# Kernel tuning notes

Measured on AMD Instinct MI355X. Metric: run time of the kernel, lower is better.

The kernel has to match this reference:

```python
import jax, jax.numpy as jnp
import numpy as np


def _lstm_step(x, h, c, wx, wh, b):
    # Keras LSTMCell gate order: i, f, g(candidate), o
    z = x @ wx + h @ wh + b
    i, f, g, o = jnp.split(z, 4, axis=-1)
    c2 = jax.nn.sigmoid(f) * c + jax.nn.sigmoid(i) * jnp.tanh(g)
    h2 = jax.nn.sigmoid(o) * jnp.tanh(c2)
    return h2, c2


def setup_inputs() -> dict:
    key = jax.random.key(0)
    ks = jax.random.split(key, 16)
    B, S, T = 64, 256, 500
    n_mel, E, P, A, D, AD, F, K = 80, 512, 256, 1024, 1024, 128, 32, 31
    g = lambda i, shape, s=0.02: jax.random.normal(ks[i], shape, jnp.float32) * s
    return {
        'memory': g(0, (B, S, E), 1.0),
        'mel_inputs': g(1, (B, T, n_mel), 1.0),
        'prenet_w1': g(2, (n_mel, P)),
        'prenet_w2': g(3, (P, P)),
        'att_lstm_wx': g(4, (P + E, 4 * A)),
        'att_lstm_wh': g(5, (A, 4 * A)),
        'att_lstm_b': jnp.zeros((4 * A,), jnp.float32),
        'w_query': g(6, (A, AD)),
        'w_memory': g(7, (E, AD)),
        'loc_conv': g(8, (K, 2, F)),
        'w_loc': g(9, (F, AD)),
        'v_att': g(10, (AD,)),
        'dec_lstm_wx': g(11, (A + E, 4 * D)),
        'dec_lstm_wh': g(12, (D, 4 * D)),
        'dec_lstm_b': jnp.zeros((4 * D,), jnp.float32),
        'proj_w': g(13, (D + E, n_mel)),
        'proj_b': jnp.zeros((n_mel,), jnp.float32),
        'gate_w': g(14, (D + E, 1)),
        'gate_b': jnp.zeros((1,), jnp.float32),
    }


def reference(memory, mel_inputs, prenet_w1, prenet_w2,
              att_lstm_wx, att_lstm_wh, att_lstm_b,
              w_query, w_memory, loc_conv, w_loc, v_att,
              dec_lstm_wx, dec_lstm_wh, dec_lstm_b,
              proj_w, proj_b, gate_w, gate_b):
    B, S, E = memory.shape
    A = att_lstm_wh.shape[0]
    D = dec_lstm_wh.shape[0]
    # keys computed once (memory layer of LSA)
    keys = memory @ w_memory  # [B, S, AD]

    def step(carry, mel_in):
        h_a, c_a, h_d, c_d, ctx, w, w_cum = carry
        # Prenet (deterministic: dropout disabled, no bias, relu)
        p = jax.nn.relu(jax.nn.relu(mel_in @ prenet_w1) @ prenet_w2)
        # Attention RNN
        x = jnp.concatenate([p, ctx], axis=-1)
        h_a, c_a = _lstm_step(x, h_a, c_a, att_lstm_wx, att_lstm_wh, att_lstm_b)
        # Location-sensitive attention
        loc = jnp.stack([w, w_cum], axis=-1)  # [B, S, 2]
        f = jax.lax.conv_general_dilated(
            loc, loc_conv, window_strides=(1,), padding='SAME',
            dimension_numbers=('NWC', 'WIO', 'NWC'))  # [B, S, F]
        e = jnp.tanh((h_a @ w_query)[:, None, :] + keys + f @ w_loc) @ v_att  # [B, S]
        w_new = jax.nn.softmax(e, axis=-1)
        ctx_new = jnp.einsum('bs,bse->be', w_new, memory)
        w_cum_new = w_cum + w_new
        # Decoder RNN (stacked, n=1)
        y = jnp.concatenate([h_a, ctx_new], axis=-1)
        h_d, c_d = _lstm_step(y, h_d, c_d, dec_lstm_wx, dec_lstm_wh, dec_lstm_b)
        cat = jnp.concatenate([h_d, ctx_new], axis=-1)
        mel = cat @ proj_w + proj_b
        stop = jax.nn.sigmoid(cat @ gate_w + gate_b)
        new_carry = (h_a, c_a, h_d, c_d, ctx_new, w_new, w_cum_new)
        return new_carry, (mel, stop, w_new)

    z = jnp.zeros
    carry0 = (z((B, A)), z((B, A)), z((B, D)), z((B, D)),
              z((B, E)), z((B, S)), z((B, S)))
    _, (mels, stops, aligns) = jax.lax.scan(step, carry0,
                                            jnp.swapaxes(mel_inputs, 0, 1))
    # [T,B,*] -> [B,T,*]
    return (jnp.swapaxes(mels, 0, 1), jnp.swapaxes(stops, 0, 1),
            jnp.swapaxes(aligns, 0, 1))
```

## Files before the change

kernel.cpp:

```cpp
#include <hip/hip_runtime.h>
#include <hip/hip_cooperative_groups.h>

namespace cg = cooperative_groups;

constexpr int NB   = 64;
constexpr int NS   = 256;
constexpr int NT   = 500;
constexpr int NMEL = 80;
constexpr int NE   = 512;
constexpr int NP   = 256;
constexpr int NA   = 1024;
constexpr int ND   = 1024;
constexpr int NAD  = 128;
constexpr int ZC   = 4096;
constexpr int KA   = 1792;
constexpr int KD   = 2560;
constexpr int NKA  = 11;
constexpr int NKD  = 16;
constexpr int G    = 512;

constexpr int SMN  = 5280;

constexpr int OFF_KEYST = 0;
constexpr int OFF_FL    = OFF_KEYST + NB * NAD * NS;
// ... 21 lines not shown
constexpr long M2_HA   = M2_ZDP + 2 * NB * ZC;
constexpr long M2_CA   = M2_HA + NB * NA;
constexpr long M2_HD   = M2_CA + NB * NA;
constexpr long M2_CD   = M2_HD + NB * ND;
constexpr long M2_CTX  = M2_CD + NB * ND;
constexpr long M2_WGL  = M2_CTX + 2 * NB * NE;
constexpr long M2_WCU  = M2_WGL + NB * NS;
constexpr long M2_PM1  = M2_WCU + NB * NS;
constexpr long M2_ZCNT = M2_PM1 - M2_HA;
constexpr long M2_BAR  = M2_PM1 + NB * NP;
constexpr long M2_FEND = M2_BAR + 1024;
constexpr long M2_WAT   = 0;
constexpr long M2_WDT   = M2_WAT + (long)ZC * KA;
constexpr long M2_X16A  = M2_WDT + (long)ZC * KD;
constexpr long M2_X16D  = M2_X16A + (long)NB * KA;
constexpr long M2_K16   = M2_X16D + (long)NB * KD;
constexpr long M2_FL16  = M2_K16 + (long)NB * NAD * NS;
constexpr long M2_MEM16 = M2_FL16 + (long)NB * NAD * NS;
constexpr long M2_UEND_NM = M2_MEM16;
constexpr long M2_UEND    = M2_MEM16 + (long)NB * NS * NE;
constexpr long M2_BYTES_NM = M2_FEND * 4 + M2_UEND_NM * 2;
constexpr long M2_BYTES    = M2_FEND * 4 + M2_UEND * 2;

constexpr int G3 = 256, T3 = 512;
constexpr long M3_W2   = 0;
constexpr long M3_ZA   = M3_W2 + 62 * NAD;
constexpr long M3_ZD   = M3_ZA + NB * ZC;
constexpr long M3_CTX  = M3_ZD + NB * ZC;
constexpr long M3_WGL  = M3_CTX + 2 * NB * NE;
constexpr long M3_WCU  = M3_WGL + NB * NS;
constexpr long M3_PM1  = M3_WCU + NB * NS;
constexpr long M3_BAR  = M3_PM1 + NB * NP;
constexpr long M3_FEND = M3_BAR + 1024;
constexpr long M3_WAT  = 0;
constexpr long M3_WDT  = M3_WAT + (long)ZC * KA;
constexpr long M3_X16A = M3_WDT + (long)ZC * KD;
constexpr long M3_X16D = M3_X16A + (long)NB * KA;
constexpr long M3_K16  = M3_X16D + (long)NB * KD;
constexpr long M3_FL16 = M3_K16 + (long)NB * NAD * NS;
constexpr long M3_WQ16 = M3_FL16 + (long)NB * NAD * NS;
constexpr long M3_MEMT = M3_WQ16 + (long)NA * NAD;
constexpr long M3_UEND = M3_MEMT + (long)NB * NE * NS;
constexpr long M3_BYTES = M3_FEND * 4 + M3_UEND * 2;
constexpr int  DYN_LDS  = 159744;

constexpr long MEL_BASE   = 0;
constexpr long STOP_BASE  = (long)NB * NT * NMEL;
constexpr long ALIGN_BASE = STOP_BASE + (long)NB * NT;

typedef __attribute__((ext_vector_type(8))) short bf16x8;
typedef __attribute__((ext_vector_type(4))) float f32x4;

struct Params {
  const float *memory, *mel, *pw1, *pw2, *awx, *awh, *ab, *wq, *wm,
              *lconv, *wloc, *vatt, *dwx, *dwh, *db, *projw, *projb, *gatew, *gateb;
  float *out, *ws;
};

__device__ __forceinline__ float sigm(float x) { return 1.f / (1.f + __expf(-x)); }
__device__ __forceinline__ float tanh_t(float x) {
  x = fminf(fmaxf(x, -15.f), 15.f);
  const float a = __expf(2.f * x);
  return (a - 1.f) / (a + 1.f);
}
__device__ __forceinline__ unsigned short f2bf(float x) {
  union { float f; unsigned u; } c; c.f = x;
  const unsigned r = c.u + 0x7FFFu + ((c.u >> 16) & 1u);
  return (unsigned short)(r >> 16);
}
__device__ __forceinline__ float bf2f(unsigned short v) {
  union { unsigned u; float f; } c; c.u = (unsigned)v << 16;
  return c.f;
}

__device__ __forceinline__ void gbar(unsigned* bar, int wg, int tid) {
  __syncthreads();
  if (tid == 0) {
    unsigned* gen  = bar;
    unsigned* root = bar + 32;
    unsigned* leaf = bar + 64 + (wg >> 5) * 32;
    const unsigned g = __hip_atomic_load(gen, __ATOMIC_RELAXED, __HIP_MEMORY_SCOPE_AGENT);
    __threadfence();
    const unsigned lo = __hip_atomic_fetch_add(leaf, 1u, __ATOMIC_ACQ_REL,
                                               __HIP_MEMORY_SCOPE_AGENT);
    if (lo == 31) {
      __hip_atomic_store(leaf, 0u, __ATOMIC_RELAXED, __HIP_MEMORY_SCOPE_AGENT);
      const unsigned ro = __hip_atomic_fetch_add(root, 1u, __ATOMIC_ACQ_REL,
                                                 __HIP_MEMORY_SCOPE_AGENT);
      if (ro == 15) {
        __hip_atomic_store(root, 0u, __ATOMIC_RELAXED, __HIP_MEMORY_SCOPE_AGENT);
        __hip_atomic_fetch_add(gen, 1u, __ATOMIC_ACQ_REL, __HIP_MEMORY_SCOPE_AGENT);
      }
    }
    while (__hip_atomic_load(gen, __ATOMIC_RELAXED, __HIP_MEMORY_SCOPE_AGENT) == g)
      __builtin_amdgcn_s_sleep(16);
// ... 8 lines not shown
    unsigned* gen  = bar;
    unsigned* root = bar + 32;
    unsigned* leaf = bar + 64 + (wg >> 4) * 32;
    const unsigned g = __hip_atomic_load(gen, __ATOMIC_RELAXED, __HIP_MEMORY_SCOPE_AGENT);
    __threadfence();
    const unsigned lo = __hip_atomic_fetch_add(leaf, 1u, __ATOMIC_ACQ_REL,
                                               __HIP_MEMORY_SCOPE_AGENT);
    if (lo == 15) {
      __hip_atomic_store(leaf, 0u, __ATOMIC_RELAXED, __HIP_MEMORY_SCOPE_AGENT);
      const unsigned ro = __hip_atomic_fetch_add(root, 1u, __ATOMIC_ACQ_REL,
                                                 __HIP_MEMORY_SCOPE_AGENT);
      if (ro == 15) {
        __hip_atomic_store(root, 0u, __ATOMIC_RELAXED, __HIP_MEMORY_SCOPE_AGENT);
        __hip_atomic_fetch_add(gen, 1u, __ATOMIC_ACQ_REL, __HIP_MEMORY_SCOPE_AGENT);
      }
    }
    while (__hip_atomic_load(gen, __ATOMIC_RELAXED, __HIP_MEMORY_SCOPE_AGENT) == g)
      __builtin_amdgcn_s_sleep(8);
    __threadfence();
  }
  __syncthreads();
}

__device__ void do_s1(const Params& p, float* pm1, int tnext, int wl, int tid) {
  const int col = tid;
  for (int i = 0; i < 8; ++i) {
    const int b = wl * 8 + i;
    const float* mrow = p.mel + ((size_t)b * NT + tnext) * NMEL;
    float acc = 0.f;
    for (int k = 0; k < NMEL; ++k) acc += mrow[k] * p.pw1[k * NP + col];
    pm1[b * NP + col] = fmaxf(acc, 0.f);
  }
}

template<int MODE>
__device__ void do_s2(const Params& p, const float* pm1, float* pdst,
                      unsigned short* xA, int wl, int tid) {
  const int col = tid;
  for (int i = 0; i < 4; ++i) {
    const int b = wl * 4 + i;
    const float* pr = pm1 + b * NP;
    float acc = 0.f;
    for (int k = 0; k < NP; ++k) acc += pr[k] * p.pw2[k * NP + col];
    const float v = fmaxf(acc, 0.f);
    if constexpr (MODE >= 2) xA[(size_t)b * KA + col] = f2bf(v);
    else                     pdst[b * NP + col] = v;
  }
}

__device__ void do_fl3(const Params& p, float* scr, unsigned short* u16, int wg, int tid) {
  float* ws = p.ws;
  float* chunk = scr;
  float* wp = scr + 3968;
  const int hf = tid >> 8, ts = tid & 255;
  const int b = (wg - 144) * 2 + hf;
  float* wp0 = wp + hf * 576;
  float* wp1 = wp0 + 288;
  for (int i = ts; i < 288; i += 256) { wp0[i] = 0.f; wp1[i] = 0.f; }
  __syncthreads();
  wp0[15 + ts] = ws[M3_WGL + b * NS + ts];
  wp1[15 + ts] = ws[M3_WCU + b * NS + ts];
  __syncthreads();
  float x0[31], x1[31];
#pragma unroll
  for (int k = 0; k < 31; ++k) { x0[k] = wp0[ts + k]; x1[k] = wp1[ts + k]; }
  const unsigned short* kb16 = u16 + M3_K16 + (size_t)(b * NAD) * NS + ts;
  unsigned short* fb16 = u16 + M3_FL16 + (size_t)(b * NAD) * NS + ts;
  const float* W2g = ws + M3_W2;
  for (int ch = 0; ch < 2; ++ch) {
    for (int i = tid; i < 62 * 64; i += T3) {
      const int k2 = i >> 6, adl = i & 63;
      chunk[i] = W2g[k2 * NAD + ch * 64 + adl];
    }
    __syncthreads();
    for (int adl = 0; adl < 64; ++adl) {
      const int ad = ch * 64 + adl;
      float acc = bf2f(kb16[(size_t)ad * NS]);
#pragma unroll
      for (int k = 0; k < 31; ++k)
        acc = fmaf(x0[k], chunk[(2 * k) * 64 + adl],
              fmaf(x1[k], chunk[(2 * k + 1) * 64 + adl], acc));
      fb16[(size_t)ad * NS] = f2bf(acc);
    }
    __syncthreads();
  }
}

__device__ void attn3(const Params& p, float* scr, unsigned short* u16,
                      int b, int tid, int t, float& c0, float& c1) {
  if (t >= NT) return;
  float* ws = p.ws;
  float* h_sh = scr;
  float* red  = scr + 1024;
  float* q_sh = scr + 1536;
  float* w_sh = scr + 1664;
  unsigned short* xA = u16 + M3_X16A + (size_t)b * KA;
  unsigned short* xD = u16 + M3_X16D + (size_t)b * KD;
  const float* za = ws + M3_ZA + (size_t)b * ZC;
#pragma unroll
  for (int j = 0; j < 2; ++j) {
    const int g = tid + j * 512;
    const float zi = p.ab[g] + za[g];
    const float zf = p.ab[1024 + g] + za[1024 + g];
    const float zg = p.ab[2048 + g] + za[2048 + g];
    const float zo = p.ab[3072 + g] + za[3072 + g];
    float& cc = j ? c1 : c0;
    const float iv = sigm(zi), fv = sigm(zf), gv = tanh_t(zg), ov = sigm(zo);
    const float cn = fv * cc + iv * gv;
    const float h2 = ov * tanh_t(cn);
    cc = cn;
    h_sh[g] = h2;
    xA[768 + g] = f2bf(h2);
    xD[g]       = f2bf(h2);
  }
  __syncthreads();
  {
    const int ad = tid & 127, kh = tid >> 7;
    const unsigned short* wqp = u16 + M3_WQ16 + ad;
    float acc = 0.f;
#pragma unroll 16
    for (int k = kh * 256; k < kh * 256 + 256; ++k) acc += h_sh[k] * bf2f(wqp[(size_t)k * NAD]);
    red[tid] = acc;
  }
  __syncthreads();
  if (tid < 128) q_sh[tid] = red[tid] + red[tid + 128] + red[tid + 256] + red[tid + 384];
  __syncthreads();
  float evp = 0.f;
  {
    const int s = tid & 255, hf = tid >> 8;
    const unsigned short* flp = u16 + M3_FL16 + (size_t)(b * NAD + hf * 64) * NS + s;
    const float* qs = q_sh + hf * 64;
    const float* va = p.vatt + hf * 64;
#pragma unroll 8
    for (int ad = 0; ad < 64; ++ad)
      evp += tanh_t(qs[ad] + bf2f(flp[(size_t)ad * NS])) * va[ad];
  }
  red[tid] = evp;
  __syncthreads();
  float evs = 0.f;
  if (tid < 256) evs = red[tid] + red[tid + 256];
  __syncthreads();
  if (tid < 256) red[tid] = evs;
  __syncthreads();
  for (int off = 128; off > 0; off >>= 1) {
    if (tid < off) red[tid] = fmaxf(red[tid], red[tid + off]);
    __syncthreads();
  }
  const float mx = red[0];
  __syncthreads();
  const float ex = (tid < 256) ? __expf(evs - mx) : 0.f;
  red[tid] = ex;
  __syncthreads();
  for (int off = 128; off > 0; off >>= 1) {
    if (tid < off) red[tid] += red[tid + off];
    __syncthreads();
  }
  const float sden = red[0];
  if (tid < 256) {
    const float wv = ex / sden;
    w_sh[tid] = wv;
    ws[M3_WGL + b * NS + tid] = wv;
    ws[M3_WCU + b * NS + tid] += wv;
    p.out[ALIGN_BASE + (size_t)b * NT * NS + (size_t)t * NS + tid] = wv;
  }
  __syncthreads();
  {
    const int e = tid;
    const unsigned short* mrow = u16 + M3_MEMT + ((size_t)b * NE + e) * NS;
    float a0 = 0.f;
#pragma unroll 4
    for (int sc = 0; sc < 32; ++sc) {
      const bf16x8 v = *(const bf16x8*)(mrow + sc * 8);
#pragma unroll
      for (int j = 0; j < 8; ++j) a0 += w_sh[sc * 8 + j] * bf2f((unsigned short)v[j]);
    }
    float* cdst = ws + M3_CTX + (t & 1) * (NB * NE) + b * NE;
    cdst[e] = a0;
    xA[256 + e]  = f2bf(a0);
    xD[1024 + e] = f2bf(a0);
  }
}

__device__ void dec3(const Params& p, float* scr, unsigned short* u16,
                     int b, int tid, int t, float& c0, float& c1) {
  if (t < 1) return;
  const int tm1 = t - 1;
  float* ws = p.ws;
  float* h_sh = scr;
  float* red  = scr + 1024;
  unsigned short* xD = u16 + M3_X16D + (size_t)b * KD;
  const float* zd = ws + M3_ZD + (size_t)b * ZC;
#pragma unroll
  for (int j = 0; j < 2; ++j) {
    const int g = tid + j * 512;
    const float zi = p.db[g] + zd[g];
    const float zf = p.db[1024 + g] + zd[1024 + g];
    const float zg = p.db[2048 + g] + zd[2048 + g];
    const float zo = p.db[3072 + g] + zd[3072 + g];
    float& cc = j ? c1 : c0;
    const float iv = sigm(zi), fv = sigm(zf), gv = tanh_t(zg), ov = sigm(zo);
    const float cn = fv * cc + iv * gv;
    const float h2 = ov * tanh_t(cn);
    cc = cn;
    h_sh[g] = h2;
    xD[1536 + g] = f2bf(h2);
  }
  __syncthreads();
  const float* ctxf = ws + M3_CTX + (tm1 & 1) * (NB * NE) + b * NE;
  red[tid] = h_sh[tid] * p.gatew[tid] + h_sh[tid + 512] * p.gatew[tid + 512]
           + ctxf[tid] * p.gatew[tid + 1024];
  __syncthreads();
  for (int off = 256; off > 0; off >>= 1) {
    if (tid < off) red[tid] += red[tid + off];
    __syncthreads();
  }
  if (tid == 0) p.out[STOP_BASE + (size_t)b * NT + tm1] = sigm(red[0] + p.gateb[0]);
  __syncthreads();
  if (tid < 480) {
    const int m = tid % 80, kh = tid / 80;
    float acc = 0.f;
#pragma unroll 8
    for (int k = kh * 256; k < kh * 256 + 256; ++k) {
      const float v = (k < 1024) ? h_sh[k] : ctxf[k - 1024];
      acc += v * p.projw[(size_t)k * 80 + m];
    }
    red[kh * 80 + m] = acc;
  }
  __syncthreads();
  if (tid < 80) {
    float mval = p.projb[tid];
#pragma unroll
    for (int kh = 0; kh < 6; ++kh) mval += red[kh * 80 + tid];
    p.out[MEL_BASE + (size_t)b * NT * NMEL + (size_t)tm1 * NMEL + tid] = mval;
  }
}

__global__ __launch_bounds__(512, 1) void taco3(Params p) {
  cg::grid_group grid = cg::this_grid();
  const int wg = blockIdx.x, tid = threadIdx.x;
  extern __shared__ char dynsm[];
  unsigned short* wA_l = (unsigned short*)dynsm;
  unsigned short* wD_l = (unsigned short*)(dynsm + 57344);
  float* scr = (float*)(dynsm + 139264);
  float* ws = p.ws;
  unsigned short* u16 = (unsigned short*)(ws + M3_FEND);

  {
    const long gid = (long)wg * T3 + tid, gstr = (long)G3 * T3;
    for (long i = gid; i < 98304; i += gstr) ws[M3_CTX + i] = 0.f;
    if (wg == 0) for (int i = tid; i < 1024; i += T3) ((unsigned*)(ws + M3_BAR))[i] = 0;
    for (long i = gid; i < 62 * NAD; i += gstr) {
      const int k2 = (int)(i >> 7), ad = (int)(i & 127);
      float a = 0.f;
      for (int f = 0; f < 32; ++f) a += p.lconv[k2 * 32 + f] * p.wloc[f * NAD + ad];
      ws[M3_W2 + i] = a;
    }
    for (long i = gid; i < (long)NB * KA + (long)NB * KD; i += gstr) u16[M3_X16A + i] = 0;
    for (long i = gid; i < (long)NA * NAD; i += gstr) u16[M3_WQ16 + i] = f2bf(p.wq[i]);
    for (long i = gid; i < (long)NB * NE * NS; i += gstr) {
      const int s = (int)(i & 255);
      const long be = i >> 8;
      const int e = (int)(be & 511), b = (int)(be >> 9);
      u16[M3_MEMT + i] = f2bf(p.memory[((size_t)b * NS + s) * NE + e]);
    }
    {
      const int b = wg >> 2, s0 = (wg & 3) * 64;
      const int sl = tid & 31, adg = tid >> 5;
      const float* wmb = p.wm + adg * 8;
      for (int so = 0; so < 64; so += 32) {
        const float* mrow = p.memory + (size_t)(b * NS + s0 + so + sl) * NE;
        float acc[8];
#pragma unroll
        for (int j = 0; j < 8; ++j) acc[j] = 0.f;
        for (int k = 0; k < NE; ++k) {
          const float mv = mrow[k];
          const float* wr = wmb + (size_t)k * NAD;
#pragma unroll
          for (int j = 0; j < 8; ++j) acc[j] += mv * wr[j];
        }
#pragma unroll
        for (int j = 0; j < 8; ++j)
          u16[M3_K16 + (size_t)(b * NAD + adg * 8 + j) * NS + s0 + so + sl] = f2bf(acc[j]);
      }
    }
    for (int tile = wg; tile < 3584 + 5120; tile += G3) {
      const bool iA = tile < 3584;
      const int tt = iA ? tile : tile - 3584;
      const int NKB = iA ? 56 : 80;
      const int nt4 = tt / NKB, kb = tt % NKB;
      const int kx = iA ? 768 : 1536;
      float4 v0{}, v1{};
      if (tid < 256) {
        const int r = tid >> 3, cgp = (tid & 7) * 8;
        const int k = kb * 32 + r;
        const float* src = iA
            ? (k < kx ? p.awx + (size_t)k * ZC : p.awh + (size_t)(k - kx) * ZC)
            : (k < kx ? p.dwx + (size_t)k * ZC : p.dwh + (size_t)(k - kx) * ZC);
        const float* sp = src + nt4 * 64 + cgp;
        v0 = *(const float4*)sp;
        v1 = *(const float4*)(sp + 4);
      }
      __syncthreads();
      if (tid < 256) {
        const int r = tid >> 3, cgp = (tid & 7) * 8;
        *(float4*)(scr + r * 64 + cgp)     = v0;
        *(float4*)(scr + r * 64 + cgp + 4) = v1;
      }
      __syncthreads();
      if (tid < 256) {
        const int blk = tid >> 6, l = tid & 63;
        const int n16 = nt4 * 4 + blk;
        bf16x8 pk;
#pragma unroll
        for (int j = 0; j < 8; ++j)
          pk[j] = (short)f2bf(scr[((l >> 4) * 8 + j) * 64 + blk * 16 + (l & 15)]);
        unsigned short* dst = u16 + (iA ? M3_WAT : M3_WDT)
                            + ((size_t)(n16 * NKB + kb)) * 512 + l * 8;
        *(bf16x8*)dst = pk;
      }
      __syncthreads();
    }
    if (wg >= 176 && wg < 184 && tid < 256) do_s1(p, ws + M3_PM1, 0, wg - 176, tid);
  }
  grid.sync();
  {
    const float4* srcA = (const float4*)(u16 + M3_WAT + (size_t)wg * 56 * 512);
    float4* dA = (float4*)wA_l;
    for (int i = tid; i < 3584; i += T3) dA[i] = srcA[i];
    const float4* srcD = (const float4*)(u16 + M3_WDT + (size_t)wg * 80 * 512);
    float4* dD = (float4*)wD_l;
    for (int i = tid; i < 5120; i += T3) dD[i] = srcD[i];
    if (wg >= 128 && wg < 144 && tid < 256)
      do_s2<3>(p, ws + M3_PM1, nullptr, u16 + M3_X16A, wg - 128, tid);
  }
  grid.sync();

  float c0 = 0.f, c1 = 0.f;
  unsigned* bar = (unsigned*)(ws + M3_BAR);
  for (int t = 0; t <= NT; ++t) {
    {
      const int wid = tid >> 6, l = tid & 63;
      if (wid < 4) {
        if (t < NT) {
          const unsigned short* xb = u16 + M3_X16A
              + (size_t)(wid * 16 + (l & 15)) * KA + (l >> 4) * 8;
          f32x4 acc{0.f, 0.f, 0.f, 0.f};
#pragma unroll 8
          for (int ks = 0; ks < 56; ++ks) {
            const bf16x8 bfr = *(const bf16x8*)(wA_l + ks * 512 + l * 8);
            const bf16x8 a   = *(const bf16x8*)(xb + ks * 32);
            acc = __builtin_amdgcn_mfma_f32_16x16x32_bf16(a, bfr, acc, 0, 0, 0);
          }
          const int ncol = wg * 16 + (l & 15), rb = (l >> 4) * 4;
          float* z = ws + M3_ZA;
#pragma unroll
          for (int r = 0; r < 4; ++r) z[(size_t)(wid * 16 + rb + r) * ZC + ncol] = acc[r];
        }
      } else {
        if (t >= 1) {
          const int mb = wid - 4;
          const unsigned short* xb = u16 + M3_X16D
              + (size_t)(mb * 16 + (l & 15)) * KD + (l >> 4) * 8;
          f32x4 acc{0.f, 0.f, 0.f, 0.f};
#pragma unroll 8
          for (int ks = 0; ks < 80; ++ks) {
            const bf16x8 bfr = *(const bf16x8*)(wD_l + ks * 512 + l * 8);
            const bf16x8 a   = *(const bf16x8*)(xb + ks * 32);
            acc = __builtin_amdgcn_mfma_f32_16x16x32_bf16(a, bfr, acc, 0, 0, 0);
          }
          const int ncol = wg * 16 + (l & 15), rb = (l >> 4) * 4;
          float* z = ws + M3_ZD;
#pragma unroll
          for (int r = 0; r < 4; ++r) z[(size_t)(mb * 16 + rb + r) * ZC + ncol] = acc[r];
        }
      }
      if (wg >= 144 && wg < 176) {
        if (t < NT) do_fl3(p, scr, u16, wg, tid);
      } else if (wg >= 176 && wg < 184) {
        if (t + 1 < NT && tid < 256) do_s1(p, ws + M3_PM1, t + 1, wg - 176, tid);
      }
    }
    gbar3(bar, wg, tid);
    if (wg < 64)       attn3(p, scr, u16, wg, tid, t, c0, c1);
    else if (wg < 128) dec3(p, scr, u16, wg - 64, tid, t, c0, c1);
    else if (wg < 144) {
      if (t + 1 < NT && tid < 256)
        do_s2<3>(p, ws + M3_PM1, nullptr, u16 + M3_X16A, wg - 128, tid);
    }
    gbar3(bar, wg, tid);
  }
}

template<bool USEMEM>
__device__ void pre_a2(const Params& p, float* sm, int wg, int tid) {
  float* ws = p.ws;
  unsigned short* u16 = (unsigned short*)(ws + M2_FEND);
  const long gid = wg * 256 + tid;
  const long gstr = (long)G * 256;
  for (long i = gid; i < M2_ZCNT; i += gstr) (ws + M2_HA)[i] = 0.f;
  if (wg == 0) for (int i = tid; i < 1024; i += 256) ((unsigned*)(ws + M2_BAR))[i] = 0;
  for (long i = gid; i < 62 * NAD; i += gstr) {
    const int k2 = (int)(i >> 7), ad = (int)(i & 127);
    float acc = 0.f;
    for (int f = 0; f < 32; ++f) acc += p.lconv[k2 * 32 + f] * p.wloc[f * NAD + ad];
    ws[M2_W2 + i] = acc;
  }
  {
    const int b = wg >> 3, s0 = (wg & 7) * 32;
    const int sl = tid & 31, adg = tid >> 5;
    const float* mrow = p.memory + (size_t)(b * NS + s0 + sl) * NE;
// ... 25 lines not shown
    const int kx = iA ? 768 : 1536;
    const int r = tid >> 3, cgp = (tid & 7) * 8;
    const int k = kb * 32 + r;
    const float* src = iA
        ? (k < kx ? p.awx + (size_t)k * ZC : p.awh + (size_t)(k - kx) * ZC)
        : (k < kx ? p.dwx + (size_t)k * ZC : p.dwh + (size_t)(k - kx) * ZC);
    const float* sp = src + nt4 * 64 + cgp;
    const float4 v0 = *(const float4*)sp;
    const float4 v1 = *(const float4*)(sp + 4);
    __syncthreads();
    *(float4*)(sm + r * 64 + cgp)     = v0;
    *(float4*)(sm + r * 64 + cgp + 4) = v1;
    __syncthreads();
    const int blk = tid >> 6, l = tid & 63;
    const int n16 = nt4 * 4 + blk;
    bf16x8 pk;
#pragma unroll
    for (int j = 0; j < 8; ++j)
      pk[j] = (short)f2bf(sm[((l >> 4) * 8 + j) * 64 + blk * 16 + (l & 15)]);
    unsigned short* dst = u16 + (iA ? M2_WAT : M2_WDT)
                        + ((size_t)(n16 * NKB + kb)) * 512 + l * 8;
    *(bf16x8*)dst = pk;
  }
  if (wg >= 320 && wg < 328) do_s1(p, ws + M2_PM1, 0, wg - 320, tid);
}

__device__ void do_fl2(const Params& p, float* sm, int b, int tid) {
  float* ws = p.ws;
  unsigned short* u16 = (unsigned short*)(ws + M2_FEND);
  float* chunk = sm;
  float* wp0 = sm + 4000;
  float* wp1 = sm + 4320;
  for (int i = tid; i < 288; i += 256) { wp0[i] = 0.f; wp1[i] = 0.f; }
  __syncthreads();
  wp0[15 + tid] = ws[M2_WGL + b * NS + tid];
  wp1[15 + tid] = ws[M2_WCU + b * NS + tid];
  __syncthreads();
  float x0[31], x1[31];
#pragma unroll
  for (int k = 0; k < 31; ++k) { x0[k] = wp0[tid + k]; x1[k] = wp1[tid + k]; }
  const unsigned short* kb16 = u16 + M2_K16 + (size_t)(b * NAD) * NS + tid;
  unsigned short* fb16 = u16 + M2_FL16 + (size_t)(b * NAD) * NS + tid;
  const float* W2g = ws + M2_W2;
  for (int ch = 0; ch < 2; ++ch) {
    for (int i = tid; i < 62 * 64; i += 256) {
      const int k2 = i >> 6, adl = i & 63;
      chunk[i] = W2g[k2 * NAD + ch * 64 + adl];
// ... 37 lines not shown
#pragma unroll 4
      for (int ks = 0; ks < nks; ++ks) {
        const bf16x8 bfr = *(const bf16x8*)(wb + (size_t)ks * 512);
        const bf16x8 a0 = *(const bf16x8*)(xb + ks * 32);
        const bf16x8 a1 = *(const bf16x8*)(xb + ks * 32 + (size_t)16 * Kp);
        const bf16x8 a2 = *(const bf16x8*)(xb + ks * 32 + (size_t)32 * Kp);
        const bf16x8 a3 = *(const bf16x8*)(xb + ks * 32 + (size_t)48 * Kp);
        acc[0] = __builtin_amdgcn_mfma_f32_16x16x32_bf16(a0, bfr, acc[0], 0, 0, 0);
        acc[1] = __builtin_amdgcn_mfma_f32_16x16x32_bf16(a1, bfr, acc[1], 0, 0, 0);
        acc[2] = __builtin_amdgcn_mfma_f32_16x16x32_bf16(a2, bfr, acc[2], 0, 0, 0);
        acc[3] = __builtin_amdgcn_mfma_f32_16x16x32_bf16(a3, bfr, acc[3], 0, 0, 0);
      }
      const int ncol = n16 * 16 + (l & 15);
      const int rb = (l >> 4) * 4;
#pragma unroll
      for (int mb = 0; mb < 4; ++mb)
#pragma unroll
        for (int r = 0; r < 4; ++r)
          zout[(size_t)(mb * 16 + rb + r) * ZC + ncol] = acc[mb][r];
    }
  } else if (wg < 320) {
    if (t < NT) do_fl2(p, sm, wg - 256, tid);
  } else if (wg < 328) {
    if (t + 1 < NT) do_s1(p, ws + M2_PM1, t + 1, wg - 320, tid);
  }
}

template<bool USEMEM>
__device__ void phase2_2(const Params& p, float* sm, int wg, int tid, int t) {
  float* ws = p.ws;
  unsigned short* u16 = (unsigned short*)(ws + M2_FEND);
  if (wg < 64) {
    if (t < NT) {
      const int b = wg;
      float* h_sh = sm;
      float* q_sh = sm + 1024;
      float* red  = sm + 1152;
      float* w_sh = sm + 1408;
      float* c_a  = ws + M2_CA;
      float* h_a  = ws + M2_HA;
      unsigned short* xA = u16 + M2_X16A + (size_t)b * KA;
      unsigned short* xD = u16 + M2_X16D + (size_t)b * KD;
      const float* za0 = ws + M2_ZAP + (size_t)b * ZC;
      const float* za1 = za0 + (size_t)NB * ZC;
#pragma unroll
      for (int j = 0; j < 4; ++j) {
        const int g = tid + j * 256;
// ... 180 lines not shown
    const int k2 = i >> 7, ad = i & 127;
    float acc = 0.f;
    for (int f = 0; f < 32; ++f) acc += p.lconv[k2 * 32 + f] * p.wloc[f * NAD + ad];
    ws[OFF_W2 + i] = acc;
  }
  {
    const int b = wg >> 3, s0 = (wg & 7) * 32;
    const int sl = tid & 31, adg = tid >> 5;
    const float* mrow = p.memory + (size_t)(b * NS + s0 + sl) * NE;
    const float* wmb  = p.wm + adg * 16;
    float acc[16];
#pragma unroll
    for (int j = 0; j < 16; ++j) acc[j] = 0.f;
    for (int k = 0; k < NE; ++k) {
      const float mv = mrow[k];
      const float* wr = wmb + (size_t)k * NAD;
#pragma unroll
      for (int j = 0; j < 16; ++j) acc[j] += mv * wr[j];
    }
#pragma unroll
    for (int j = 0; j < 16; ++j)
      ws[OFF_KEYST + (b * NAD + adg * 16 + j) * NS + s0 + sl] = acc[j];
  }
  if (wg >= 496 && wg < 504) do_s1(p, ws + OFF_PM1, 0, wg - 496, tid);
}

__device__ void do_fl(const Params& p, float* sm, int b, int tid) {
  float* ws = p.ws;
  float* chunk = sm;
  float* wp0 = sm + 4000;
  float* wp1 = sm + 4320;
  for (int i = tid; i < 288; i += 256) { wp0[i] = 0.f; wp1[i] = 0.f; }
  __syncthreads();
  wp0[15 + tid] = ws[OFF_WGL + b * NS + tid];
  wp1[15 + tid] = ws[OFF_WCU + b * NS + tid];
  __syncthreads();
  float x0[31], x1[31];
#pragma unroll
  for (int k = 0; k < 31; ++k) { x0[k] = wp0[tid + k]; x1[k] = wp1[tid + k]; }
  const float* kb = ws + OFF_KEYST + (b * NAD) * NS + tid;
  float* fb = ws + OFF_FL + (b * NAD) * NS + tid;
  const float* W2g = ws + OFF_W2;
  for (int ch = 0; ch < 2; ++ch) {
    for (int i = tid; i < 62 * 64; i += 256) {
      const int k2 = i >> 6, adl = i & 63;
      chunk[i] = W2g[k2 * NAD + ch * 64 + adl];
    }
// ... 126 lines not shown
      if constexpr (MODE == 1) {
        float* zdp = ws + OFF_ZDP;
#pragma unroll
        for (int i = 0; i < 8; ++i) {
          const int b = b0 + bgrp * 8 + i;
          float* dst = zdp + (size_t)(kci * NB + b) * ZC + c;
          *(float4*)dst       = make_float4(acc[i][0], acc[i][1], acc[i][2], acc[i][3]);
          *(float4*)(dst + 4) = make_float4(acc[i][4], acc[i][5], acc[i][6], acc[i][7]);
        }
      } else {
        float* z_d = ws + OFF_ZD;
#pragma unroll
        for (int i = 0; i < 8; ++i) {
          const int b = b0 + bgrp * 8 + i;
#pragma unroll
          for (int j = 0; j < 8; ++j) atomicAdd(&z_d[b * ZC + c + j], acc[i][j]);
        }
      }
      __syncthreads();
    }
  } else if (wg < 496) {
    if (t < NT) do_fl(p, sm, wg - 432, tid);
  } else if (wg < 504) {
    if (t + 1 < NT) do_s1(p, ws + OFF_PM1, t + 1, wg - 496, tid);
  }
}

template<int MODE>
__device__ void phase2(const Params& p, float* sm, int wg, int tid, int t) {
  float* ws = p.ws;
  if (wg < 64) {
    if (t < NT) {
      const int b = wg;
      float* h_sh = sm;
      float* q_sh = sm + 1024;
      float* red  = sm + 1152;
      float* w_sh = sm + 1408;
      float* c_a  = ws + OFF_CA;
      float* h_a  = ws + OFF_HA;
#pragma unroll
      for (int j = 0; j < 4; ++j) {
        const int g = tid + j * 256;
        float zi, zf, zg, zo;
        if constexpr (MODE == 1) {
          zi = p.ab[g]; zf = p.ab[1024 + g]; zg = p.ab[2048 + g]; zo = p.ab[3072 + g];
          const float* zap = ws + OFF_ZAP + (size_t)b * ZC;
#pragma unroll 1
// ... 189 lines not shown
  prm.mel    = (const float*)d_in[1];
  prm.pw1    = (const float*)d_in[2];
  prm.pw2    = (const float*)d_in[3];
  prm.awx    = (const float*)d_in[4];
  prm.awh    = (const float*)d_in[5];
  prm.ab     = (const float*)d_in[6];
  prm.wq     = (const float*)d_in[7];
  prm.wm     = (const float*)d_in[8];
  prm.lconv  = (const float*)d_in[9];
  prm.wloc   = (const float*)d_in[10];
  prm.vatt   = (const float*)d_in[11];
  prm.dwx    = (const float*)d_in[12];
  prm.dwh    = (const float*)d_in[13];
  prm.db     = (const float*)d_in[14];
  prm.projw  = (const float*)d_in[15];
  prm.projb  = (const float*)d_in[16];
  prm.gatew  = (const float*)d_in[17];
  prm.gateb  = (const float*)d_in[18];
  prm.out = (float*)d_out;
  prm.ws  = (float*)d_ws;

  void* args[] = { &prm };
  hipError_t err = hipErrorUnknown;
  if (ws_size >= (size_t)M3_BYTES) {
    (void)hipFuncSetAttribute((const void*)taco3,
                              hipFuncAttributeMaxDynamicSharedMemorySize, DYN_LDS);
    err = hipLaunchCooperativeKernel((void*)taco3, dim3(G3), dim3(T3),
                                     args, DYN_LDS, stream);
  }
  if (err != hipSuccess && ws_size >= (size_t)M2_BYTES)
    err = hipLaunchCooperativeKernel((void*)taco2<true>, dim3(G), dim3(256), args, 0, stream);
  if (err != hipSuccess && ws_size >= (size_t)M2_BYTES_NM)
    err = hipLaunchCooperativeKernel((void*)taco2<false>, dim3(G), dim3(256), args, 0, stream);
  if (err != hipSuccess && ws_size >= (size_t)WS_FULL * sizeof(float))
    err = hipLaunchCooperativeKernel((void*)taco_coop<1>, dim3(G), dim3(256), args, 0, stream);
  if (err != hipSuccess)
    err = hipLaunchCooperativeKernel((void*)taco_coop<0>, dim3(G), dim3(256), args, 0, stream);
  if (err != hipSuccess) {
    k_pre_a<<<dim3(G), dim3(256), 0, stream>>>(prm);
    k_pre_b<<<dim3(G), dim3(256), 0, stream>>>(prm);
    for (int t = 0; t <= NT; ++t) {
      k_p1<<<dim3(G), dim3(256), 0, stream>>>(prm, t);
      k_p2<<<dim3(G), dim3(256), 0, stream>>>(prm, t);
    }
  }
}
```

Before: 97.25 ms.

## Transpose keys, location features, query and projection weights for vectorized contiguous access

Stores keys and location features as [B,S,AD] so each thread reads and writes 8 contiguous bf16 values with vector loads, rather than strided scalar accesses. Also pre-transposes w_query and proj_w in setup so the query and mel-projection dot products read contiguous memory, and raises unroll factors on the MFMA and context loops. Adds atomic-load/store helpers for a new MODE 4 that nothing calls yet. The setup phase gains two extra transposition passes and the workspace grows slightly.

```diff
diff --git a/kernel.cpp b/kernel.cpp
--- a/kernel.cpp
+++ b/kernel.cpp
@@ -67,26 +67,27 @@
 constexpr long M2_BYTES_NM = M2_FEND * 4 + M2_UEND_NM * 2;
 constexpr long M2_BYTES    = M2_FEND * 4 + M2_UEND * 2;
 
-constexpr int G3 = 256, T3 = 512;
-constexpr long M3_W2   = 0;
-constexpr long M3_ZA   = M3_W2 + 62 * NAD;
-constexpr long M3_ZD   = M3_ZA + NB * ZC;
-constexpr long M3_CTX  = M3_ZD + NB * ZC;
-constexpr long M3_WGL  = M3_CTX + 2 * NB * NE;
-constexpr long M3_WCU  = M3_WGL + NB * NS;
-constexpr long M3_PM1  = M3_WCU + NB * NS;
-constexpr long M3_BAR  = M3_PM1 + NB * NP;
-constexpr long M3_FEND = M3_BAR + 1024;
-constexpr long M3_WAT  = 0;
-constexpr long M3_WDT  = M3_WAT + (long)ZC * KA;
-constexpr long M3_X16A = M3_WDT + (long)ZC * KD;
-constexpr long M3_X16D = M3_X16A + (long)NB * KA;
-constexpr long M3_K16  = M3_X16D + (long)NB * KD;
-constexpr long M3_FL16 = M3_K16 + (long)NB * NAD * NS;
-constexpr long M3_WQ16 = M3_FL16 + (long)NB * NAD * NS;
-constexpr long M3_MEMT = M3_WQ16 + (long)NA * NAD;
-constexpr long M3_UEND = M3_MEMT + (long)NB * NE * NS;
-constexpr long M3_BYTES = M3_FEND * 4 + M3_UEND * 2;
+constexpr int G5 = 256, T5 = 512;
+constexpr long M5_W2     = 0;
+constexpr long M5_ZA     = M5_W2 + 62 * NAD;
+constexpr long M5_ZD     = M5_ZA + NB * ZC;
+constexpr long M5_CTX    = M5_ZD + NB * ZC;
+constexpr long M5_WGL    = M5_CTX + 2 * NB * NE;
+constexpr long M5_WCU    = M5_WGL + NB * NS;
+constexpr long M5_PM1    = M5_WCU + NB * NS;
+constexpr long M5_PROJWT = M5_PM1 + NB * NP;
+constexpr long M5_BAR    = M5_PROJWT + 80 * 1536;
+constexpr long M5_FEND   = M5_BAR + 1024;
+constexpr long M5_WAT   = 0;
+constexpr long M5_WDT   = M5_WAT + (long)ZC * KA;
+constexpr long M5_X16A  = M5_WDT + (long)ZC * KD;
+constexpr long M5_X16D  = M5_X16A + (long)NB * KA;
+constexpr long M5_K16T  = M5_X16D + (long)NB * KD;
+constexpr long M5_FL16T = M5_K16T + (long)NB * NS * NAD;
+constexpr long M5_WQT   = M5_FL16T + (long)NB * NS * NAD;
+constexpr long M5_MEMT  = M5_WQT + (long)NAD * NA;
+constexpr long M5_UEND  = M5_MEMT + (long)NB * NE * NS;
+constexpr long M5_BYTES = M5_FEND * 4 + M5_UEND * 2;
 constexpr int  DYN_LDS  = 159744;
 
 constexpr long MEL_BASE   = 0;
@@ -116,6 +117,15 @@
 __device__ __forceinline__ float bf2f(unsigned short v) {
   union { unsigned u; float f; } c; c.u = (unsigned)v << 16;
   return c.f;
+}
+__device__ __forceinline__ float ldf(const float* p) {
+  return __hip_atomic_load(p, __ATOMIC_RELAXED, __HIP_MEMORY_SCOPE_AGENT);
+}
+__device__ __forceinline__ void stf(float* p, float v) {
+  __hip_atomic_store(p, v, __ATOMIC_RELAXED, __HIP_MEMORY_SCOPE_AGENT);
+}
+__device__ __forceinline__ void stw(unsigned short* p, unsigned short v) {
+  __hip_atomic_store(p, v, __ATOMIC_RELAXED, __HIP_MEMORY_SCOPE_AGENT);
 }
 
 __device__ __forceinline__ void gbar(unsigned* bar, int wg, int tid) {
@@ -170,6 +180,7 @@
   __syncthreads();
 }
 
+template<int MODE>
 __device__ void do_s1(const Params& p, float* pm1, int tnext, int wl, int tid) {
   const int col = tid;
   for (int i = 0; i < 8; ++i) {
@@ -177,7 +188,8 @@
     const float* mrow = p.mel + ((size_t)b * NT + tnext) * NMEL;
     float acc = 0.f;
     for (int k = 0; k < NMEL; ++k) acc += mrow[k] * p.pw1[k * NP + col];
-    pm1[b * NP + col] = fmaxf(acc, 0.f);
+    if constexpr (MODE == 4) stf(&pm1[b * NP + col], fmaxf(acc, 0.f));
+    else                     pm1[b * NP + col] = fmaxf(acc, 0.f);
   }
 }
 
@@ -189,52 +201,67 @@
     const int b = wl * 4 + i;
     const float* pr = pm1 + b * NP;
     float acc = 0.f;
-    for (int k = 0; k < NP; ++k) acc += pr[k] * p.pw2[k * NP + col];
+    if constexpr (MODE == 4) {
+      for (int k = 0; k < NP; ++k) acc += ldf(&pr[k]) * p.pw2[k * NP + col];
+    } else {
+      for (int k = 0; k < NP; ++k) acc += pr[k] * p.pw2[k * NP + col];
+    }
     const float v = fmaxf(acc, 0.f);
-    if constexpr (MODE >= 2) xA[(size_t)b * KA + col] = f2bf(v);
-    else                     pdst[b * NP + col] = v;
-  }
-}
-
-__device__ void do_fl3(const Params& p, float* scr, unsigned short* u16, int wg, int tid) {
+    if constexpr (MODE == 4)      stw(&xA[(size_t)b * KA + col], f2bf(v));
+    else if constexpr (MODE >= 2) xA[(size_t)b * KA + col] = f2bf(v);
+    else                          pdst[b * NP + col] = v;
+  }
+}
+
+__device__ void do_fl5(const Params& p, float* scr, unsigned short* u16, int wg, int tid) {
   float* ws = p.ws;
   float* chunk = scr;
   float* wp = scr + 3968;
-  const int hf = tid >> 8, ts = tid & 255;
+  const int hf = tid >> 8, s = tid & 255;
   const int b = (wg - 144) * 2 + hf;
   float* wp0 = wp + hf * 576;
   float* wp1 = wp0 + 288;
-  for (int i = ts; i < 288; i += 256) { wp0[i] = 0.f; wp1[i] = 0.f; }
-  __syncthreads();
-  wp0[15 + ts] = ws[M3_WGL + b * NS + ts];
-  wp1[15 + ts] = ws[M3_WCU + b * NS + ts];
+  for (int i = s; i < 288; i += 256) { wp0[i] = 0.f; wp1[i] = 0.f; }
+  __syncthreads();
+  wp0[15 + s] = ws[M5_WGL + b * NS + s];
+  wp1[15 + s] = ws[M5_WCU + b * NS + s];
   __syncthreads();
   float x0[31], x1[31];
 #pragma unroll
-  for (int k = 0; k < 31; ++k) { x0[k] = wp0[ts + k]; x1[k] = wp1[ts + k]; }
-  const unsigned short* kb16 = u16 + M3_K16 + (size_t)(b * NAD) * NS + ts;
-  unsigned short* fb16 = u16 + M3_FL16 + (size_t)(b * NAD) * NS + ts;
-  const float* W2g = ws + M3_W2;
+  for (int k = 0; k < 31; ++k) { x0[k] = wp0[s + k]; x1[k] = wp1[s + k]; }
+  const unsigned short* kb = u16 + M5_K16T + ((size_t)(b * NS + s)) * NAD;
+  unsigned short* fb = u16 + M5_FL16T + ((size_t)(b * NS + s)) * NAD;
+  const float* W2g = ws + M5_W2;
   for (int ch = 0; ch < 2; ++ch) {
-    for (int i = tid; i < 62 * 64; i += T3) {
+    for (int i = tid; i < 62 * 64; i += T5) {
       const int k2 = i >> 6, adl = i & 63;
       chunk[i] = W2g[k2 * NAD + ch * 64 + adl];
     }
     __syncthreads();
-    for (int adl = 0; adl < 64; ++adl) {
-      const int ad = ch * 64 + adl;
-      float acc = bf2f(kb16[(size_t)ad * NS]);
-#pragma unroll
-      for (int k = 0; k < 31; ++k)
-        acc = fmaf(x0[k], chunk[(2 * k) * 64 + adl],
-              fmaf(x1[k], chunk[(2 * k + 1) * 64 + adl], acc));
-      fb16[(size_t)ad * NS] = f2bf(acc);
+#pragma unroll
+    for (int blk = 0; blk < 8; ++blk) {
+      const bf16x8 kv = *(const bf16x8*)(kb + ch * 64 + blk * 8);
+      float acc[8];
+#pragma unroll
+      for (int j = 0; j < 8; ++j) acc[j] = bf2f((unsigned short)kv[j]);
+#pragma unroll
+      for (int k = 0; k < 31; ++k) {
+        const float* c0p = chunk + (2 * k) * 64 + blk * 8;
+        const float* c1p = chunk + (2 * k + 1) * 64 + blk * 8;
+#pragma unroll
+        for (int j = 0; j < 8; ++j)
+          acc[j] = fmaf(x0[k], c0p[j], fmaf(x1[k], c1p[j], acc[j]));
+      }
+      bf16x8 pk;
+#pragma unroll
+      for (int j = 0; j < 8; ++j) pk[j] = (short)f2bf(acc[j]);
+      *(bf16x8*)(fb + ch * 64 + blk * 8) = pk;
     }
     __syncthreads();
   }
 }
 
-__device__ void attn3(const Params& p, float* scr, unsigned short* u16,
+__device__ void attn5(const Params& p, float* scr, unsigned short* u16,
                       int b, int tid, int t, float& c0, float& c1) {
   if (t >= NT) return;
   float* ws = p.ws;
@@ -242,9 +269,9 @@
   float* red  = scr + 1024;
   float* q_sh = scr + 1536;
   float* w_sh = scr + 1664;
-  unsigned short* xA = u16 + M3_X16A + (size_t)b * KA;
-  unsigned short* xD = u16 + M3_X16D + (size_t)b * KD;
-  const float* za = ws + M3_ZA + (size_t)b * ZC;
+  unsigned short* xA = u16 + M5_X16A + (size_t)b * KA;
+  unsigned short* xD = u16 + M5_X16D + (size_t)b * KD;
+  const float* za = ws + M5_ZA + (size_t)b * ZC;
 #pragma unroll
   for (int j = 0; j < 2; ++j) {
     const int g = tid + j * 512;
@@ -264,10 +291,15 @@
   __syncthreads();
   {
     const int ad = tid & 127, kh = tid >> 7;
-    const unsigned short* wqp = u16 + M3_WQ16 + ad;
+    const unsigned short* wqp = u16 + M5_WQT + (size_t)ad * NA + kh * 256;
+    const float* hp = h_sh + kh * 256;
     float acc = 0.f;
-#pragma unroll 16
-    for (int k = kh * 256; k < kh * 256 + 256; ++k) acc += h_sh[k] * bf2f(wqp[(size_t)k * NAD]);
+#pragma unroll 8
+    for (int c8 = 0; c8 < 32; ++c8) {
+      const bf16x8 v = *(const bf16x8*)(wqp + c8 * 8);
+#pragma unroll
+      for (int j = 0; j < 8; ++j) acc += hp[c8 * 8 + j] * bf2f((unsigned short)v[j]);
+    }
     red[tid] = acc;
   }
   __syncthreads();
@@ -276,12 +308,16 @@
   float evp = 0.f;
   {
     const int s = tid & 255, hf = tid >> 8;
-    const unsigned short* flp = u16 + M3_FL16 + (size_t)(b * NAD + hf * 64) * NS + s;
+    const unsigned short* flp = u16 + M5_FL16T + ((size_t)(b * NS + s)) * NAD + hf * 64;
     const float* qs = q_sh + hf * 64;
     const float* va = p.vatt + hf * 64;
-#pragma unroll 8
-    for (int ad = 0; ad < 64; ++ad)
-      evp += tanh_t(qs[ad] + bf2f(flp[(size_t)ad * NS])) * va[ad];
+#pragma unroll
+    for (int blk = 0; blk < 8; ++blk) {
+      const bf16x8 v = *(const bf16x8*)(flp + blk * 8);
+#pragma unroll
+      for (int j = 0; j < 8; ++j)
+        evp += tanh_t(qs[blk * 8 + j] + bf2f((unsigned short)v[j])) * va[blk * 8 + j];
+    }
   }
   red[tid] = evp;
   __syncthreads();
@@ -307,37 +343,37 @@
   if (tid < 256) {
     const float wv = ex / sden;
     w_sh[tid] = wv;
-    ws[M3_WGL + b * NS + tid] = wv;
-    ws[M3_WCU + b * NS + tid] += wv;
+    ws[M5_WGL + b * NS + tid] = wv;
+    ws[M5_WCU + b * NS + tid] += wv;
     p.out[ALIGN_BASE + (size_t)b * NT * NS + (size_t)t * NS + tid] = wv;
   }
   __syncthreads();
   {
     const int e = tid;
-    const unsigned short* mrow = u16 + M3_MEMT + ((size_t)b * NE + e) * NS;
+    const unsigned short* mrow = u16 + M5_MEMT + ((size_t)b * NE + e) * NS;
     float a0 = 0.f;
-#pragma unroll 4
+#pragma unroll 16
     for (int sc = 0; sc < 32; ++sc) {
       const bf16x8 v = *(const bf16x8*)(mrow + sc * 8);
 #pragma unroll
       for (int j = 0; j < 8; ++j) a0 += w_sh[sc * 8 + j] * bf2f((unsigned short)v[j]);
     }
-    float* cdst = ws + M3_CTX + (t & 1) * (NB * NE) + b * NE;
+    float* cdst = ws + M5_CTX + (t & 1) * (NB * NE) + b * NE;
     cdst[e] = a0;
     xA[256 + e]  = f2bf(a0);
     xD[1024 + e] = f2bf(a0);
   }
 }
 
-__device__ void dec3(const Params& p, float* scr, unsigned short* u16,
+__device__ void dec5(const Params& p, float* scr, unsigned short* u16,
                      int b, int tid, int t, float& c0, float& c1) {
   if (t < 1) return;
   const int tm1 = t - 1;
   float* ws = p.ws;
   float* h_sh = scr;
   float* red  = scr + 1024;
-  unsigned short* xD = u16 + M3_X16D + (size_t)b * KD;
-  const float* zd = ws + M3_ZD + (size_t)b * ZC;
+  unsigned short* xD = u16 + M5_X16D + (size_t)b * KD;
+  const float* zd = ws + M5_ZD + (size_t)b * ZC;
 #pragma unroll
   for (int j = 0; j < 2; ++j) {
     const int g = tid + j * 512;
@@ -354,7 +390,7 @@
     xD[1536 + g] = f2bf(h2);
   }
   __syncthreads();
-  const float* ctxf = ws + M3_CTX + (tm1 & 1) * (NB * NE) + b * NE;
+  const float* ctxf = ws + M5_CTX + (tm1 & 1) * (NB * NE) + b * NE;
   red[tid] = h_sh[tid] * p.gatew[tid] + h_sh[tid + 512] * p.gatew[tid + 512]
            + ctxf[tid] * p.gatew[tid + 1024];
   __syncthreads();
@@ -366,11 +402,13 @@
   __syncthreads();
   if (tid < 480) {
     const int m = tid % 80, kh = tid / 80;
+    const float* pw = ws + M5_PROJWT + (size_t)m * 1536 + kh * 256;
     float acc = 0.f;
 #pragma unroll 8
-    for (int k = kh * 256; k < kh * 256 + 256; ++k) {
-      const float v = (k < 1024) ? h_sh[k] : ctxf[k - 1024];
-      acc += v * p.projw[(size_t)k * 80 + m];
+    for (int k = 0; k < 256; ++k) {
+      const int kk = kh * 256 + k;
+      const float v = (kk < 1024) ? h_sh[kk] : ctxf[kk - 1024];
+      acc += v * pw[k];
     }
     red[kh * 80 + m] = acc;
   }
@@ -383,7 +421,7 @@
   }
 }
 
-__global__ __launch_bounds__(512, 1) void taco3(Params p) {
+__global__ __launch_bounds__(512, 1) void taco5(Params p) {
   cg::grid_group grid = cg::this_grid();
   const int wg = blockIdx.x, tid = threadIdx.x;
   extern __shared__ char dynsm[];
@@ -391,25 +429,32 @@
   unsigned short* wD_l = (unsigned short*)(dynsm + 57344);
   float* scr = (float*)(dynsm + 139264);
   float* ws = p.ws;
-  unsigned short* u16 = (unsigned short*)(ws + M3_FEND);
+  unsigned short* u16 = (unsigned short*)(ws + M5_FEND);
 
   {
-    const long gid = (long)wg * T3 + tid, gstr = (long)G3 * T3;
-    for (long i = gid; i < 98304; i += gstr) ws[M3_CTX + i] = 0.f;
-    if (wg == 0) for (int i = tid; i < 1024; i += T3) ((unsigned*)(ws + M3_BAR))[i] = 0;
+    const long gid = (long)wg * T5 + tid, gstr = (long)G5 * T5;
+    for (long i = gid; i < 98304; i += gstr) ws[M5_CTX + i] = 0.f;
+    if (wg == 0) for (int i = tid; i < 1024; i += T5) ((unsigned*)(ws + M5_BAR))[i] = 0;
     for (long i = gid; i < 62 * NAD; i += gstr) {
       const int k2 = (int)(i >> 7), ad = (int)(i & 127);
       float a = 0.f;
       for (int f = 0; f < 32; ++f) a += p.lconv[k2 * 32 + f] * p.wloc[f * NAD + ad];
-      ws[M3_W2 + i] = a;
-    }
-    for (long i = gid; i < (long)NB * KA + (long)NB * KD; i += gstr) u16[M3_X16A + i] = 0;
-    for (long i = gid; i < (long)NA * NAD; i += gstr) u16[M3_WQ16 + i] = f2bf(p.wq[i]);
+      ws[M5_W2 + i] = a;
+    }
+    for (long i = gid; i < (long)NB * KA + (long)NB * KD; i += gstr) u16[M5_X16A + i] = 0;
+    for (long i = gid; i < (long)NAD * NA; i += gstr) {
+      const int ad = (int)(i >> 10), k = (int)(i & 1023);
+      u16[M5_WQT + i] = f2bf(p.wq[(size_t)k * NAD + ad]);
+    }
+    for (long i = gid; i < (long)80 * 1536; i += gstr) {
+      const int m = (int)(i / 1536), k = (int)(i % 1536);
+      ws[M5_PROJWT + i] = p.projw[(size_t)k * 80 + m];
+    }
     for (long i = gid; i < (long)NB * NE * NS; i += gstr) {
       const int s = (int)(i & 255);
       const long be = i >> 8;
       const int e = (int)(be & 511), b = (int)(be >> 9);
-      u16[M3_MEMT + i] = f2bf(p.memory[((size_t)b * NS + s) * NE + e]);
+      u16[M5_MEMT + i] = f2bf(p.memory[((size_t)b * NS + s) * NE + e]);
     }
     {
       const int b = wg >> 2, s0 = (wg & 3) * 64;
@@ -426,12 +471,13 @@
 #pragma unroll
           for (int j = 0; j < 8; ++j) acc[j] += mv * wr[j];
         }
-#pragma unroll
-        for (int j = 0; j < 8; ++j)
-          u16[M3_K16 + (size_t)(b * NAD + adg * 8 + j) * NS + s0 + so + sl] = f2bf(acc[j]);
-      }
-    }
-    for (int tile = wg; tile < 3584 + 5120; tile += G3) {
+        bf16x8 pk;
+#pragma unroll
+        for (int j = 0; j < 8; ++j) pk[j] = (short)f2bf(acc[j]);
+        *(bf16x8*)(u16 + M5_K16T + ((size_t)(b * NS + s0 + so + sl)) * NAD + adg * 8) = pk;
+      }
+    }
+    for (int tile = wg; tile < 3584 + 5120; tile += G5) {
       const bool iA = tile < 3584;
       const int tt = iA ? tile : tile - 3584;
       const int NKB = iA ? 56 : 80;
@@ -462,78 +508,78 @@
 #pragma unroll
         for (int j = 0; j < 8; ++j)
           pk[j] = (short)f2bf(scr[((l >> 4) * 8 + j) * 64 + blk * 16 + (l & 15)]);
-        unsigned short* dst = u16 + (iA ? M3_WAT : M3_WDT)
+        unsigned short* dst = u16 + (iA ? M5_WAT : M5_WDT)
                             + ((size_t)(n16 * NKB + kb)) * 512 + l * 8;
         *(bf16x8*)dst = pk;
       }
       __syncthreads();
     }
-    if (wg >= 176 && wg < 184 && tid < 256) do_s1(p, ws + M3_PM1, 0, wg - 176, tid);
+    if (wg >= 176 && wg < 184 && tid < 256) do_s1<3>(p, ws + M5_PM1, 0, wg - 176, tid);
   }
   grid.sync();
   {
-    const float4* srcA = (const float4*)(u16 + M3_WAT + (size_t)wg * 56 * 512);
+    const float4* srcA = (const float4*)(u16 + M5_WAT + (size_t)wg * 56 * 512);
     float4* dA = (float4*)wA_l;
-    for (int i = tid; i < 3584; i += T3) dA[i] = srcA[i];
-    const float4* srcD = (const float4*)(u16 + M3_WDT + (size_t)wg * 80 * 512);
+    for (int i = tid; i < 3584; i += T5) dA[i] = srcA[i];
+    const float4* srcD = (const float4*)(u16 + M5_WDT + (size_t)wg * 80 * 512);
     float4* dD = (float4*)wD_l;
-    for (int i = tid; i < 5120; i += T3) dD[i] = srcD[i];
+    for (int i = tid; i < 5120; i += T5) dD[i] = srcD[i];
     if (wg >= 128 && wg < 144 && tid < 256)
-      do_s2<3>(p, ws + M3_PM1, nullptr, u16 + M3_X16A, wg - 128, tid);
+      do_s2<3>(p, ws + M5_PM1, nullptr, u16 + M5_X16A, wg - 128, tid);
   }
   grid.sync();
 
   float c0 = 0.f, c1 = 0.f;
-  unsigned* bar = (unsigned*)(ws + M3_BAR);
+  unsigned* bar = (unsigned*)(ws + M5_BAR);
   for (int t = 0; t <= NT; ++t) {
     {
       const int wid = tid >> 6, l = tid & 63;
       if (wid < 4) {
         if (t < NT) {
-          const unsigned short* xb = u16 + M3_X16A
+          const unsigned short* xb = u16 + M5_X16A
               + (size_t)(wid * 16 + (l & 15)) * KA + (l >> 4) * 8;
           f32x4 acc{0.f, 0.f, 0.f, 0.f};
-#pragma unroll 8
+#pragma unroll 16
           for (int ks = 0; ks < 56; ++ks) {
             const bf16x8 bfr = *(const bf16x8*)(wA_l + ks * 512 + l * 8);
             const bf16x8 a   = *(const bf16x8*)(xb + ks * 32);
             acc = __builtin_amdgcn_mfma_f32_16x16x32_bf16(a, bfr, acc, 0, 0, 0);
           }
           const int ncol = wg * 16 + (l & 15), rb = (l >> 4) * 4;
-          float* z = ws + M3_ZA;
+          float* z = ws + M5_ZA;
 #pragma unroll
           for (int r = 0; r < 4; ++r) z[(size_t)(wid * 16 + rb + r) * ZC + ncol] = acc[r];
         }
       } else {
         if (t >= 1) {
           const int mb = wid - 4;
-          const unsigned short* xb = u16 + M3_X16D
+          const unsigned short* xb = u16 + M5_X16D
               + (size_t)(mb * 16 + (l & 15)) * KD + (l >> 4) * 8;
           f32x4 acc{0.f, 0.f, 0.f, 0.f};
-#pragma unroll 8
+#pragma unroll 16
           for (int ks = 0; ks < 80; ++ks) {
             const bf16x8 bfr = *(const bf16x8*)(wD_l + ks * 512 + l * 8);
             const bf16x8 a   = *(const bf16x8*)(xb + ks * 32);
             acc = __builtin_amdgcn_mfma_f32_16x16x32_bf16(a, bfr, acc, 0, 0, 0);
           }
           const int ncol = wg * 16 + (l & 15), rb = (l >> 4) * 4;
-          float* z = ws + M3_ZD;
+          float* z = ws + M5_ZD;
 #pragma unroll
           for (int r = 0; r < 4; ++r) z[(size_t)(mb * 16 + rb + r) * ZC + ncol] = acc[r];
         }
       }
       if (wg >= 144 && wg < 176) {
-        if (t < NT) do_fl3(p, scr, u16, wg, tid);
+        if (t < NT) do_fl5(p, scr, u16, wg, tid);
       } else if (wg >= 176 && wg < 184) {
-        if (t + 1 < NT && tid < 256) do_s1(p, ws + M3_PM1, t + 1, wg - 176, tid);
+        if (t + 1 < NT && tid < 256) do_s1<3>(p, ws + M5_PM1, t + 1, wg - 176, tid);
       }
     }
     gbar3(bar, wg, tid);
-    if (wg < 64)       attn3(p, scr, u16, wg, tid, t, c0, c1);
-    else if (wg < 128) dec3(p, scr, u16, wg - 64, tid, t, c0, c1);
+    if (wg < 64)       attn5(p, scr, u16, wg, tid, t, c0, c1);
+    else if (wg < 128) dec5(p, scr, u16, wg - 64, tid, t, c0, c1);
     else if (wg < 144) {
       if (t + 1 < NT && tid < 256)
-        do_s2<3>(p, ws + M3_PM1, nullptr, u16 + M3_X16A, wg - 128, tid);
+        do_s2<3>(p, ws + M5_PM1, nullptr, u16 + M5_X16A, wg - 128, tid);
     }
     gbar3(bar, wg, tid);
   }
@@ -605,7 +651,7 @@
                         + ((size_t)(n16 * NKB + kb)) * 512 + l * 8;
     *(bf16x8*)dst = pk;
   }
-  if (wg >= 320 && wg < 328) do_s1(p, ws + M2_PM1, 0, wg - 320, tid);
+  if (wg >= 320 && wg < 328) do_s1<2>(p, ws + M2_PM1, 0, wg - 320, tid);
 }
 
 __device__ void do_fl2(const Params& p, float* sm, int b, int tid) {
@@ -689,7 +735,7 @@
   } else if (wg < 320) {
     if (t < NT) do_fl2(p, sm, wg - 256, tid);
   } else if (wg < 328) {
-    if (t + 1 < NT) do_s1(p, ws + M2_PM1, t + 1, wg - 320, tid);
+    if (t + 1 < NT) do_s1<2>(p, ws + M2_PM1, t + 1, wg - 320, tid);
   }
 }
 
@@ -916,7 +962,7 @@
     for (int j = 0; j < 16; ++j)
       ws[OFF_KEYST + (b * NAD + adg * 16 + j) * NS + s0 + sl] = acc[j];
   }
-  if (wg >= 496 && wg < 504) do_s1(p, ws + OFF_PM1, 0, wg - 496, tid);
+  if (wg >= 496 && wg < 504) do_s1<0>(p, ws + OFF_PM1, 0, wg - 496, tid);
 }
 
 __device__ void do_fl(const Params& p, float* sm, int b, int tid) {
@@ -1089,7 +1135,7 @@
   } else if (wg < 496) {
     if (t < NT) do_fl(p, sm, wg - 432, tid);
   } else if (wg < 504) {
-    if (t + 1 < NT) do_s1(p, ws + OFF_PM1, t + 1, wg - 496, tid);
+    if (t + 1 < NT) do_s1<0>(p, ws + OFF_PM1, t + 1, wg - 496, tid);
   }
 }
 
@@ -1325,10 +1371,10 @@
 
   void* args[] = { &prm };
   hipError_t err = hipErrorUnknown;
-  if (ws_size >= (size_t)M3_BYTES) {
-    (void)hipFuncSetAttribute((const void*)taco3,
+  if (ws_size >= (size_t)M5_BYTES) {
+    (void)hipFuncSetAttribute((const void*)taco5,
                               hipFuncAttributeMaxDynamicSharedMemorySize, DYN_LDS);
-    err = hipLaunchCooperativeKernel((void*)taco3, dim3(G3), dim3(T3),
+    err = hipLaunchCooperativeKernel((void*)taco5, dim3(G5), dim3(T5),
                                      args, DYN_LDS, stream);
   }
   if (err != hipSuccess && ws_size >= (size_t)M2_BYTES)
```

Result: slower. 151.7 ms (+56.0%).
